# Kernel optimization log

Measured on AMD Instinct MI355X. Metric: run time of the kernel, lower is better.

## Reference

```python
import jax, jax.numpy as jnp
import numpy as np

K = 12
ORDERS = [(1, 2, 3), (1, 3, 2), (3, 2, 1), (3, 1, 2), (2, 1, 3), (2, 3, 1)]


def ranking_3d(x):
    # x: (B, L1, W1, H1, D) -> (B, 12, L1*W1*H1, D)
    B, L1, W1, H1, D = x.shape
    seqs = []
    for dims in ORDERS:
        perm = (0,) + dims + (4,)
        seqs.append(jnp.transpose(x, perm).reshape(B, -1, D))
        xr = jnp.flip(x, axis=dims)
        seqs.append(jnp.transpose(xr, perm).reshape(B, -1, D))
    return jnp.stack(seqs, axis=1)


def restore_original(out_y, shape):
    # out_y: (B, 12, D, L). NOTE: faithfully replicates the original code, which
    # reshapes the (B, D, L) slice directly to (B, d1, d2, d3, D).
    B, L1, W1, H1, D = shape
    size = {1: L1, 2: W1, 3: H1}
    restored = []
    for i in range(12):
        dims = ORDERS[i // 2]
        seq = out_y[:, i]  # (B, D, L)
        dims_shape = tuple(size[d] for d in dims)
        reshaped = seq.reshape((B,) + dims_shape + (D,))
        perm = (0,) + dims + (4,)
        inv = tuple(np.argsort(perm))
        r = jnp.transpose(reshaped, inv)
        if i % 2 == 1:
            r = jnp.flip(r, axis=dims)
        restored.append(r)
    return restored


def selective_scan(u, delta, A, Bs, Cs):
    # u, delta: (B,K,D,L); A: (K,D,N); Bs, Cs: (B,K,N,L)
    us = jnp.moveaxis(u, -1, 0)       # (L,B,K,D)
    ds = jnp.moveaxis(delta, -1, 0)   # (L,B,K,D)
    Bts = jnp.moveaxis(Bs, -1, 0)     # (L,B,K,N)
    Cts = jnp.moveaxis(Cs, -1, 0)     # (L,B,K,N)
    h0 = jnp.zeros(u.shape[:-1] + (A.shape[-1],), u.dtype)  # (B,K,D,N)

    def step(h, inp):
        ut, dt, Bt, Ct = inp
        dA = jnp.exp(dt[..., None] * A)                       # (B,K,D,N)
        h = dA * h + (dt * ut)[..., None] * Bt[:, :, None, :]
        y = jnp.einsum('bkdn,bkn->bkd', h, Ct)
        return h, y

    _, ys = jax.lax.scan(step, h0, (us, ds, Bts, Cts))
    return jnp.moveaxis(ys, 0, -1)  # (B,K,D,L)


def setup_inputs() -> dict:
    key = jax.random.key(0)
    ks = jax.random.split(key, 8)
    B, H, W, Len, D = 1, 16, 16, 16, 128
    N, R = 16, 8
    x = jax.random.normal(ks[0], (B, H, W, Len, D), dtype=jnp.float32)
    x_proj_weight = jax.random.normal(ks[1], (K, R + 2 * N, D), dtype=jnp.float32) * 0.02
    std = R ** -0.5
    dt_projs_weight = jax.random.uniform(ks[2], (K, D, R), minval=-std, maxval=std, dtype=jnp.float32)
    dt = jnp.exp(jax.random.uniform(ks[3], (K, D)) * (np.log(0.1) - np.log(0.001)) + np.log(0.001))
    dt = jnp.clip(dt, 1e-4, None)
    dt_projs_bias = (dt + jnp.log(-jnp.expm1(-dt))).astype(jnp.float32)
    A_logs = jnp.broadcast_to(jnp.log(jnp.arange(1, N + 1, dtype=jnp.float32)), (K, D, N)).copy()
    Ds = jnp.ones((K, D), dtype=jnp.float32)
    merge_w = jax.random.normal(ks[4], (K,), dtype=jnp.float32) * (1.0 / K)
    merge_b = jax.random.normal(ks[5], (), dtype=jnp.float32) * 0.01
    return {'x': x, 'x_proj_weight': x_proj_weight, 'dt_projs_weight': dt_projs_weight,
            'dt_projs_bias': dt_projs_bias, 'A_logs': A_logs, 'Ds': Ds,
            'merge_w': merge_w, 'merge_b': merge_b}


def reference(x, x_proj_weight, dt_projs_weight, dt_projs_bias, A_logs, Ds, merge_w, merge_b):
    B, H, W, Len, D = x.shape
    L = H * W * Len
    R = dt_projs_weight.shape[-1]
    N = A_logs.shape[-1]
    xs = jnp.transpose(ranking_3d(x), (0, 1, 3, 2))  # (B,K,D,L)
    x_dbl = jnp.einsum('bkdl,kcd->bkcl', xs, x_proj_weight)  # (B,K,R+2N,L)
    dts, Bs, Cs = jnp.split(x_dbl, [R, R + N], axis=2)
    dts = jnp.einsum('bkrl,kdr->bkdl', dts, dt_projs_weight)
    delta = jax.nn.softplus(dts + dt_projs_bias[None, :, :, None])
    A = -jnp.exp(A_logs)  # (K,D,N)
    ys = selective_scan(xs, delta, A, Bs, Cs)
    out_y = ys + Ds[None, :, :, None] * xs  # (B,K,D,L)
    restored = restore_original(out_y, (B, H, W, Len, D))
    stacked = jnp.stack(restored, axis=1)  # (B,K,H,W,Len,D)
    # mergeconv: 1x1 Conv2d over K channels == weighted sum across directions
    y = jnp.einsum('bkhwld,k->bhwld', stacked, merge_w) + merge_b
    return y
```

## Files before the change

### kernel.cpp

```cpp
#include <hip/hip_runtime.h>

#define KK 12
#define LL 4096
#define DD 128
#define NN 16
#define RR 8
#define NC 64
#define LC 64
#define XST 132
#define YST 66
#define SDST 44
#define XDBL_TILE (64 * SDST)

__device__ __forceinline__ int pos_of(int k, int l) {
    int o = k >> 1;
    int le = (k & 1) ? (4095 - l) : l;
    int t1 = le >> 8, t2 = (le >> 4) & 15, t3 = le & 15;
    switch (o) {
        case 0:  return (t1 << 8) | (t2 << 4) | t3;
        case 1:  return (t1 << 8) | (t3 << 4) | t2;
        case 2:  return (t3 << 8) | (t2 << 4) | t1;
        case 3:  return (t2 << 8) | (t3 << 4) | t1;
        case 4:  return (t2 << 8) | (t1 << 4) | t3;
        default: return (t3 << 8) | (t1 << 4) | t2;
    }
}

__device__ __forceinline__ float softplus_f(float z) {
    return fmaxf(z, 0.0f) + __logf(1.0f + __expf(-fabsf(z)));
}

__device__ __forceinline__ float delta_at(const float* sdbl, int i,
                                          float4 w0, float4 w1, float bz) {
    const float4* dr = (const float4*)(sdbl + i * SDST);
    float4 r0 = dr[0], r1 = dr[1];
    float z = bz + w0.x * r0.x + w0.y * r0.y + w0.z * r0.z + w0.w * r0.w
                 + w1.x * r1.x + w1.y * r1.y + w1.z * r1.z + w1.w * r1.w;
    return softplus_f(z);
}

__device__ __forceinline__ void e8_vec(bool structured, int half, float tl,
                                       float A0, const float* A8, float* e) {
    if (structured) {
        float q = __expf(tl * A0);
        float q2 = q * q, q4 = q2 * q2, q8 = q4 * q4;
        e[0] = half ? q8 * q : q;
        #pragma unroll
        for (int j = 1; j < 8; j++) e[j] = e[j - 1] * q;
    } else {
        #pragma unroll
        for (int j = 0; j < 8; j++) e[j] = __expf(tl * A8[j]);
    }
}

__device__ __forceinline__ bool load_A8(const float* __restrict__ A_logs,
                                        int k, int d, int n0, float* A8, float& A0) {
    const float4* ap = (const float4*)(A_logs + ((size_t)(k * DD + d) * NN + n0));
    float4 a0 = ap[0], a1 = ap[1];
    A8[0] = -__expf(a0.x); A8[1] = -__expf(a0.y);
    A8[2] = -__expf(a0.z); A8[3] = -__expf(a0.w);
    A8[4] = -__expf(a1.x); A8[5] = -__expf(a1.y);
    A8[6] = -__expf(a1.z); A8[7] = -__expf(a1.w);
    A0 = -__expf(A_logs[(size_t)(k * DD + d) * NN]);
    bool s = true;
    #pragma unroll
    for (int j = 0; j < 8; j++) {
        float m = (float)(n0 + j + 1);
        s = s && (fabsf(A8[j] - m * A0) <= 1e-4f * m * fabsf(A0));
    }
    return s;
}

__global__ __launch_bounds__(256) void k1_proj_scanA(
    const float* __restrict__ x, const float* __restrict__ Wp,
    const float* __restrict__ Wdt, const float* __restrict__ bias,
    const float* __restrict__ A_logs, const float* __restrict__ Ds,
    float* __restrict__ S, float* __restrict__ dtsum,
    float* __restrict__ oy, float* __restrict__ xdbl)
{
    const int blk = blockIdx.x;
    const int k = blk >> 6;
    const int c = blk & 63;
    const int l0 = c * LC;
    const int t = threadIdx.x;

    __shared__ float xs[64 * XST];
    __shared__ float sdbl[64 * SDST];
    __shared__ int   pos_s[64];

    if (t < 64) pos_s[t] = pos_of(k, l0 + t);
    __syncthreads();

    {
        int lane32 = t & 31, rowi = t >> 5;
        #pragma unroll
        for (int p = 0; p < 8; p++) {
            int l = p * 8 + rowi;
            float4 v = *(const float4*)(x + (size_t)pos_s[l] * DD + lane32 * 4);
            *(float4*)(&xs[l * XST + lane32 * 4]) = v;
        }
    }
    __syncthreads();

    {
        int l = t & 63, cgch = t >> 6;
        float acc[10];
        #pragma unroll
        for (int j = 0; j < 10; j++) acc[j] = 0.0f;
        const float* wk = Wp + (size_t)(k * 40 + cgch * 10) * DD;
        for (int d4 = 0; d4 < DD; d4 += 4) {
            float4 xv = *(const float4*)(&xs[l * XST + d4]);
            #pragma unroll
            for (int j = 0; j < 10; j++) {
                const float* w = wk + j * DD + d4;
                acc[j] += xv.x * w[0] + xv.y * w[1] + xv.z * w[2] + xv.w * w[3];
            }
        }
        #pragma unroll
        for (int j = 0; j < 10; j++) sdbl[l * SDST + cgch * 10 + j] = acc[j];
    }
    __syncthreads();

    if (c != 0) {
        for (int idx = t; idx < XDBL_TILE; idx += 256)
            xdbl[(size_t)blk * XDBL_TILE + idx] = sdbl[idx];
    }

    const int d = t >> 1, half = t & 1, n0 = half * 8;
    float A8[8], A0;
    bool structured = load_A8(A_logs, k, d, n0, A8, A0);
    const float4* wp4 = (const float4*)(Wdt + (size_t)(k * DD + d) * RR);
    const float4 w0 = wp4[0], w1 = wp4[1];
    const float bz = bias[k * DD + d];
    const float Dval = Ds[k * DD + d];
    float* ybuf = xs;

    {
        float h[8] = {0, 0, 0, 0, 0, 0, 0, 0};
        float dsum = 0.0f;
        #pragma unroll 4
        for (int i = 0; i < LC; i++) {
            float tl = delta_at(sdbl, i, w0, w1, bz);
            dsum += tl;
            float u = x[(size_t)pos_s[i] * DD + d];
            const float4* bp = (const float4*)(&sdbl[i * SDST + 8 + n0]);
            float4 b0 = bp[0], b1 = bp[1];
            const float4* cp = (const float4*)(&sdbl[i * SDST + 24 + n0]);
            float4 c0 = cp[0], c1 = cp[1];
            float e[8];
            e8_vec(structured, half, tl, A0, A8, e);
            float tu = tl * u;
            h[0] = e[0] * h[0] + tu * b0.x;  h[1] = e[1] * h[1] + tu * b0.y;
            h[2] = e[2] * h[2] + tu * b0.z;  h[3] = e[3] * h[3] + tu * b0.w;
            h[4] = e[4] * h[4] + tu * b1.x;  h[5] = e[5] * h[5] + tu * b1.y;
            h[6] = e[6] * h[6] + tu * b1.z;  h[7] = e[7] * h[7] + tu * b1.w;
            float yp = h[0] * c0.x + h[1] * c0.y + h[2] * c0.z + h[3] * c0.w
                     + h[4] * c1.x + h[5] * c1.y + h[6] * c1.z + h[7] * c1.w;
            float y = yp + __shfl_xor(yp, 1);
            if (!half) ybuf[d * YST + i] = y + Dval * u;
        }
        float4* sp = (float4*)(S + (((size_t)(k * NC + c) * DD + d) * NN + n0));
        sp[0] = make_float4(h[0], h[1], h[2], h[3]);
        sp[1] = make_float4(h[4], h[5], h[6], h[7]);
        if (!half) dtsum[(k * NC + c) * DD + d] = dsum;
    }
    __syncthreads();

    {
        int row = t >> 4, col = (t & 15) * 4;
        #pragma unroll
        for (int p = 0; p < 8; p++) {
            int r = p * 16 + row;
            float4 v = *(const float4*)(&ybuf[r * YST + col]);
            *(float4*)(oy + ((size_t)(k * DD + r)) * LL + l0 + col) = v;
        }
    }
}

__global__ __launch_bounds__(256) void k2_combine(
    float* __restrict__ S, const float* __restrict__ dtsum,
    const float* __restrict__ A_logs)
{
    int tid = blockIdx.x * 256 + threadIdx.x;
    int kk = tid >> 11, rem = tid & 2047, dd2 = rem >> 4;
    float Ac = -__expf(A_logs[tid]);
    float hh = 0.0f;
    #pragma unroll 8
    for (int c2 = 0; c2 < NC; c2++) {
        size_t base = ((size_t)(kk * NC + c2)) * 2048 + rem;
        float s = S[base];
        float dsv = dtsum[(kk * NC + c2) * DD + dd2];
        S[base] = hh;
        hh = s + __expf(dsv * Ac) * hh;
    }
}

__global__ __launch_bounds__(256) void k3_corr(
    const float* __restrict__ Wdt, const float* __restrict__ bias,
    const float* __restrict__ A_logs, const float* __restrict__ S,
    const float* __restrict__ xdbl, float* __restrict__ oy)
{
    const int blk = blockIdx.x;
    const int k = blk >> 6;
    const int c = blk & 63;
    if (c == 0) return;
    const int l0 = c * LC;
    const int t = threadIdx.x;

    __shared__ float sdbl[64 * SDST];
    __shared__ float ybuf[128 * YST];

    for (int idx = t; idx < XDBL_TILE; idx += 256)
        sdbl[idx] = xdbl[(size_t)blk * XDBL_TILE + idx];
    for (int idx = t; idx < 128 * YST; idx += 256)
        ybuf[idx] = 0.0f;
    __syncthreads();

    const int d = t >> 1, half = t & 1, n0 = half * 8;
    float A8[8], A0;
    bool structured = load_A8(A_logs, k, d, n0, A8, A0);
    const float4* wp4 = (const float4*)(Wdt + (size_t)(k * DD + d) * RR);
    const float4 w0 = wp4[0], w1 = wp4[1];
    const float bz = bias[k * DD + d];

    float corr[8];
    {
        const float4* hp = (const float4*)(S + (((size_t)(k * NC + c) * DD + d) * NN + n0));
        float4 h40 = hp[0], h41 = hp[1];
        corr[0] = h40.x; corr[1] = h40.y; corr[2] = h40.z; corr[3] = h40.w;
        corr[4] = h41.x; corr[5] = h41.y; corr[6] = h41.z; corr[7] = h41.w;
    }

    bool alive = true;
    for (int ii = 0; ii < 8 && alive; ii++) {
        #pragma unroll
        for (int jj = 0; jj < 8; jj++) {
            int i = ii * 8 + jj;
            float tl = delta_at(sdbl, i, w0, w1, bz);
            float e[8];
            e8_vec(structured, half, tl, A0, A8, e);
            #pragma unroll
            for (int j = 0; j < 8; j++) corr[j] *= e[j];
            const float4* cp = (const float4*)(&sdbl[i * SDST + 24 + n0]);
            float4 c0 = cp[0], c1 = cp[1];
            float yp = corr[0] * c0.x + corr[1] * c0.y + corr[2] * c0.z + corr[3] * c0.w
                     + corr[4] * c1.x + corr[5] * c1.y + corr[6] * c1.z + corr[7] * c1.w;
            float y = yp + __shfl_xor(yp, 1);
            if (!half) ybuf[d * YST + i] = y;
        }
        float mag = fabsf(corr[0]) + fabsf(corr[1]) + fabsf(corr[2]) + fabsf(corr[3])
                  + fabsf(corr[4]) + fabsf(corr[5]) + fabsf(corr[6]) + fabsf(corr[7]);
        if (__all(mag == 0.0f)) alive = false;
    }
    __syncthreads();

    {
        int row = t >> 4, col = (t & 15) * 4;
        #pragma unroll
        for (int p = 0; p < 8; p++) {
            int r = p * 16 + row;
            float4* addr = (float4*)(oy + ((size_t)(k * DD + r)) * LL + l0 + col);
            float4 v = *addr;
            const float4 w = *(const float4*)(&ybuf[r * YST + col]);
            v.x += w.x; v.y += w.y; v.z += w.z; v.w += w.w;
            *addr = v;
        }
    }
}

__global__ __launch_bounds__(256) void k4_merge(
    const float* __restrict__ out_y, const float* __restrict__ mw,
    const float* __restrict__ mb, float* __restrict__ out)
{
    int idx = blockIdx.x * 256 + threadIdx.x;
    int dd = idx & 127;
    int p = idx >> 7;
    int i3 = p & 15, i2 = (p >> 4) & 15, i1 = (p >> 8) & 15;

    float accv = mb[0];
    #pragma unroll
    for (int k = 0; k < 12; k++) {
        int a1 = i1, a2 = i2, a3 = i3;
        if (k & 1) { a1 = 15 - i1; a2 = 15 - i2; a3 = 15 - i3; }
        int j1, j2, j3;
        switch (k >> 1) {
            case 0:  j1 = a1; j2 = a2; j3 = a3; break;
            case 1:  j1 = a1; j2 = a3; j3 = a2; break;
            case 2:  j1 = a3; j2 = a2; j3 = a1; break;
            case 3:  j1 = a3; j2 = a1; j3 = a2; break;
            case 4:  j1 = a2; j2 = a1; j3 = a3; break;
            default: j1 = a2; j2 = a3; j3 = a1; break;
        }
        int jb = (j1 << 8) | (j2 << 4) | j3;
        accv += mw[k] * out_y[(size_t)k * (DD * LL) + (jb >> 5) * LL
                              + ((jb & 31) << 7) + dd];
    }
    out[idx] = accv;
}

extern "C" void kernel_launch(void* const* d_in, const int* in_sizes, int n_in,
                              void* d_out, int out_size, void* d_ws, size_t ws_size,
                              hipStream_t stream) {
    const float* x      = (const float*)d_in[0];
    const float* Wp     = (const float*)d_in[1];
    const float* Wdt    = (const float*)d_in[2];
    const float* bias   = (const float*)d_in[3];
    const float* A_logs = (const float*)d_in[4];
    const float* Ds     = (const float*)d_in[5];
    const float* mw     = (const float*)d_in[6];
    const float* mb     = (const float*)d_in[7];
    float* out = (float*)d_out;

    float* ws   = (float*)d_ws;
    float* S    = ws;
    float* dts  = S + (size_t)KK * NC * DD * NN;
    float* oy   = dts + (size_t)KK * NC * DD;
    float* xdbl = oy + (size_t)KK * DD * LL;

    k1_proj_scanA<<<dim3(KK * NC), dim3(256), 0, stream>>>(
        x, Wp, Wdt, bias, A_logs, Ds, S, dts, oy, xdbl);
    k2_combine<<<dim3(KK * DD * NN / 256), dim3(256), 0, stream>>>(S, dts, A_logs);
    k3_corr<<<dim3(KK * NC), dim3(256), 0, stream>>>(Wdt, bias, A_logs, S, xdbl, oy);
    k4_merge<<<dim3(LL * DD / 256), dim3(256), 0, stream>>>(oy, mw, mb, out);
}
```

Before: 179.3 us.

## Template scan kernels on structured A, keep outputs in registers, closed-form correction

The scan and correction kernels become templated on whether A is structured, so the per-step branch disappears and the 64-step loops fully unroll. Each thread pair keeps its half of the y outputs in registers and writes them straight to global memory, removing the shared-memory y buffer and its extra barrier. The scan now reads u from the shared x tile instead of global memory. The correction kernel computes exp(cumulative delta * A) * h0 in closed form, which removes the serial multiply chain and the early-exit test but puts an exp on every step. Launch bounds now request minimum occupancy, and copies use float4, at the risk of register spills from the larger unrolled bodies.

```diff
diff --git a/kernel.cpp b/kernel.cpp
--- a/kernel.cpp
+++ b/kernel.cpp
@@ -8,7 +8,6 @@
 #define NC 64
 #define LC 64
 #define XST 132
-#define YST 66
 #define SDST 44
 #define XDBL_TILE (64 * SDST)
 
@@ -26,31 +25,12 @@
     }
 }
 
-__device__ __forceinline__ float softplus_f(float z) {
-    return fmaxf(z, 0.0f) + __logf(1.0f + __expf(-fabsf(z)));
-}
-
-__device__ __forceinline__ float delta_at(const float* sdbl, int i,
-                                          float4 w0, float4 w1, float bz) {
+__device__ __forceinline__ float delta_row_z(const float* sdbl, int i,
+                                             float4 w0, float4 w1, float bz) {
     const float4* dr = (const float4*)(sdbl + i * SDST);
     float4 r0 = dr[0], r1 = dr[1];
-    float z = bz + w0.x * r0.x + w0.y * r0.y + w0.z * r0.z + w0.w * r0.w
-                 + w1.x * r1.x + w1.y * r1.y + w1.z * r1.z + w1.w * r1.w;
-    return softplus_f(z);
-}
-
-__device__ __forceinline__ void e8_vec(bool structured, int half, float tl,
-                                       float A0, const float* A8, float* e) {
-    if (structured) {
-        float q = __expf(tl * A0);
-        float q2 = q * q, q4 = q2 * q2, q8 = q4 * q4;
-        e[0] = half ? q8 * q : q;
-        #pragma unroll
-        for (int j = 1; j < 8; j++) e[j] = e[j - 1] * q;
-    } else {
-        #pragma unroll
-        for (int j = 0; j < 8; j++) e[j] = __expf(tl * A8[j]);
-    }
+    return bz + w0.x * r0.x + w0.y * r0.y + w0.z * r0.z + w0.w * r0.w
+              + w1.x * r1.x + w1.y * r1.y + w1.z * r1.z + w1.w * r1.w;
 }
 
 __device__ __forceinline__ bool load_A8(const float* __restrict__ A_logs,
@@ -71,11 +51,74 @@
     return s;
 }
 
-__global__ __launch_bounds__(256) void k1_proj_scanA(
+template<bool S>
+__device__ __forceinline__ void e8_from(float v, float A0, const float* A8,
+                                        int half, float* e) {
+    if (S) {
+        float q = __expf(v * A0);
+        float q2 = q * q, q4 = q2 * q2, q8 = q4 * q4;
+        e[0] = half ? q8 * q : q;
+        #pragma unroll
+        for (int j = 1; j < 8; j++) e[j] = e[j - 1] * q;
+    } else {
+        #pragma unroll
+        for (int j = 0; j < 8; j++) e[j] = __expf(v * A8[j]);
+    }
+}
+
+template<bool S>
+__device__ __forceinline__ void scanA_body(
+    const float* xs, const float* sdbl, int k, int c, int l0,
+    int d, int half, int n0, const float* A8, float A0,
+    float4 w0, float4 w1, float bz, float Dval,
+    float* __restrict__ S_g, float* __restrict__ dtsum,
+    float* __restrict__ oy)
+{
+    float h[8] = {0, 0, 0, 0, 0, 0, 0, 0};
+    float ybr[32];
+    float dsum = 0.0f;
+
+    #pragma unroll
+    for (int i = 0; i < LC; i++) {
+        float z = delta_row_z(sdbl, i, w0, w1, bz);
+        float E = __expf(-fabsf(z));
+        float dt = fmaxf(z, 0.0f) + __logf(1.0f + E);
+        float u = xs[i * XST + d];
+        dsum += dt;
+        float tu = dt * u;
+        float e[8];
+        e8_from<S>(dt, A0, A8, half, e);
+        const float4* bp = (const float4*)(&sdbl[i * SDST + 8 + n0]);
+        float4 b0 = bp[0], b1 = bp[1];
+        const float4* cp = (const float4*)(&sdbl[i * SDST + 24 + n0]);
+        float4 c0 = cp[0], c1 = cp[1];
+        h[0] = e[0] * h[0] + tu * b0.x;  h[1] = e[1] * h[1] + tu * b0.y;
+        h[2] = e[2] * h[2] + tu * b0.z;  h[3] = e[3] * h[3] + tu * b0.w;
+        h[4] = e[4] * h[4] + tu * b1.x;  h[5] = e[5] * h[5] + tu * b1.y;
+        h[6] = e[6] * h[6] + tu * b1.z;  h[7] = e[7] * h[7] + tu * b1.w;
+        float yp = h[0] * c0.x + h[1] * c0.y + h[2] * c0.z + h[3] * c0.w
+                 + h[4] * c1.x + h[5] * c1.y + h[6] * c1.z + h[7] * c1.w;
+        float yv = yp + __shfl_xor(yp, 1) + Dval * u;
+        if ((i >> 5) == half) ybr[i & 31] = yv;
+    }
+
+    float4* sp = (float4*)(S_g + (((size_t)(k * NC + c) * DD + d) * NN + n0));
+    sp[0] = make_float4(h[0], h[1], h[2], h[3]);
+    sp[1] = make_float4(h[4], h[5], h[6], h[7]);
+    if (!half) dtsum[(k * NC + c) * DD + d] = dsum;
+
+    float* base = oy + ((size_t)(k * DD + d)) * LL + l0 + half * 32;
+    #pragma unroll
+    for (int j = 0; j < 8; j++)
+        *(float4*)(base + j * 4) = make_float4(ybr[4*j], ybr[4*j+1],
+                                               ybr[4*j+2], ybr[4*j+3]);
+}
+
+__global__ __launch_bounds__(256, 3) void k1_proj_scanA(
     const float* __restrict__ x, const float* __restrict__ Wp,
     const float* __restrict__ Wdt, const float* __restrict__ bias,
     const float* __restrict__ A_logs, const float* __restrict__ Ds,
-    float* __restrict__ S, float* __restrict__ dtsum,
+    float* __restrict__ S_g, float* __restrict__ dtsum,
     float* __restrict__ oy, float* __restrict__ xdbl)
 {
     const int blk = blockIdx.x;
@@ -84,9 +127,9 @@
     const int l0 = c * LC;
     const int t = threadIdx.x;
 
-    __shared__ float xs[64 * XST];
-    __shared__ float sdbl[64 * SDST];
-    __shared__ int   pos_s[64];
+    __shared__ __align__(16) float xs[64 * XST];
+    __shared__ __align__(16) float sdbl[64 * SDST];
+    __shared__ int pos_s[64];
 
     if (t < 64) pos_s[t] = pos_of(k, l0 + t);
     __syncthreads();
@@ -122,8 +165,9 @@
     __syncthreads();
 
     if (c != 0) {
-        for (int idx = t; idx < XDBL_TILE; idx += 256)
-            xdbl[(size_t)blk * XDBL_TILE + idx] = sdbl[idx];
+        const float4* s4 = (const float4*)sdbl;
+        float4* g4 = (float4*)(xdbl + (size_t)blk * XDBL_TILE);
+        for (int idx = t; idx < XDBL_TILE / 4; idx += 256) g4[idx] = s4[idx];
     }
 
     const int d = t >> 1, half = t & 1, n0 = half * 8;
@@ -133,52 +177,17 @@
     const float4 w0 = wp4[0], w1 = wp4[1];
     const float bz = bias[k * DD + d];
     const float Dval = Ds[k * DD + d];
-    float* ybuf = xs;
-
-    {
-        float h[8] = {0, 0, 0, 0, 0, 0, 0, 0};
-        float dsum = 0.0f;
-        #pragma unroll 4
-        for (int i = 0; i < LC; i++) {
-            float tl = delta_at(sdbl, i, w0, w1, bz);
-            dsum += tl;
-            float u = x[(size_t)pos_s[i] * DD + d];
-            const float4* bp = (const float4*)(&sdbl[i * SDST + 8 + n0]);
-            float4 b0 = bp[0], b1 = bp[1];
-            const float4* cp = (const float4*)(&sdbl[i * SDST + 24 + n0]);
-            float4 c0 = cp[0], c1 = cp[1];
-            float e[8];
-            e8_vec(structured, half, tl, A0, A8, e);
-            float tu = tl * u;
-            h[0] = e[0] * h[0] + tu * b0.x;  h[1] = e[1] * h[1] + tu * b0.y;
-            h[2] = e[2] * h[2] + tu * b0.z;  h[3] = e[3] * h[3] + tu * b0.w;
-            h[4] = e[4] * h[4] + tu * b1.x;  h[5] = e[5] * h[5] + tu * b1.y;
-            h[6] = e[6] * h[6] + tu * b1.z;  h[7] = e[7] * h[7] + tu * b1.w;
-            float yp = h[0] * c0.x + h[1] * c0.y + h[2] * c0.z + h[3] * c0.w
-                     + h[4] * c1.x + h[5] * c1.y + h[6] * c1.z + h[7] * c1.w;
-            float y = yp + __shfl_xor(yp, 1);
-            if (!half) ybuf[d * YST + i] = y + Dval * u;
-        }
-        float4* sp = (float4*)(S + (((size_t)(k * NC + c) * DD + d) * NN + n0));
-        sp[0] = make_float4(h[0], h[1], h[2], h[3]);
-        sp[1] = make_float4(h[4], h[5], h[6], h[7]);
-        if (!half) dtsum[(k * NC + c) * DD + d] = dsum;
-    }
-    __syncthreads();
-
-    {
-        int row = t >> 4, col = (t & 15) * 4;
-        #pragma unroll
-        for (int p = 0; p < 8; p++) {
-            int r = p * 16 + row;
-            float4 v = *(const float4*)(&ybuf[r * YST + col]);
-            *(float4*)(oy + ((size_t)(k * DD + r)) * LL + l0 + col) = v;
-        }
-    }
+
+    if (structured)
+        scanA_body<true>(xs, sdbl, k, c, l0, d, half, n0, A8, A0, w0, w1, bz,
+                         Dval, S_g, dtsum, oy);
+    else
+        scanA_body<false>(xs, sdbl, k, c, l0, d, half, n0, A8, A0, w0, w1, bz,
+                          Dval, S_g, dtsum, oy);
 }
 
 __global__ __launch_bounds__(256) void k2_combine(
-    float* __restrict__ S, const float* __restrict__ dtsum,
+    float* __restrict__ S_g, const float* __restrict__ dtsum,
     const float* __restrict__ A_logs)
 {
     int tid = blockIdx.x * 256 + threadIdx.x;
@@ -188,16 +197,50 @@
     #pragma unroll 8
     for (int c2 = 0; c2 < NC; c2++) {
         size_t base = ((size_t)(kk * NC + c2)) * 2048 + rem;
-        float s = S[base];
+        float s = S_g[base];
         float dsv = dtsum[(kk * NC + c2) * DD + dd2];
-        S[base] = hh;
+        S_g[base] = hh;
         hh = s + __expf(dsv * Ac) * hh;
     }
 }
 
-__global__ __launch_bounds__(256) void k3_corr(
+template<bool S>
+__device__ __forceinline__ void corr_body(
+    const float* sdbl, int k, int c, int l0, int d, int half, int n0,
+    const float* A8, float A0, const float* h0,
+    float4 w0, float4 w1, float bz, float* __restrict__ oy)
+{
+    float ybr[32];
+    float Dsum = 0.0f;
+
+    #pragma unroll
+    for (int i = 0; i < LC; i++) {
+        float z = delta_row_z(sdbl, i, w0, w1, bz);
+        float E = __expf(-fabsf(z));
+        float dt = fmaxf(z, 0.0f) + __logf(1.0f + E);
+        Dsum += dt;
+        float e[8];
+        e8_from<S>(Dsum, A0, A8, half, e);
+        const float4* cp = (const float4*)(&sdbl[i * SDST + 24 + n0]);
+        float4 c0 = cp[0], c1 = cp[1];
+        float yp = e[0]*h0[0]*c0.x + e[1]*h0[1]*c0.y + e[2]*h0[2]*c0.z + e[3]*h0[3]*c0.w
+                 + e[4]*h0[4]*c1.x + e[5]*h0[5]*c1.y + e[6]*h0[6]*c1.z + e[7]*h0[7]*c1.w;
+        float yv = yp + __shfl_xor(yp, 1);
+        if ((i >> 5) == half) ybr[i & 31] = yv;
+    }
+
+    float* base = oy + ((size_t)(k * DD + d)) * LL + l0 + half * 32;
+    #pragma unroll
+    for (int j = 0; j < 8; j++) {
+        float4 v = *(float4*)(base + j * 4);
+        v.x += ybr[4*j]; v.y += ybr[4*j+1]; v.z += ybr[4*j+2]; v.w += ybr[4*j+3];
+        *(float4*)(base + j * 4) = v;
+    }
+}
+
+__global__ __launch_bounds__(256, 4) void k3_corr(
     const float* __restrict__ Wdt, const float* __restrict__ bias,
-    const float* __restrict__ A_logs, const float* __restrict__ S,
+    const float* __restrict__ A_logs, const float* __restrict__ S_g,
     const float* __restrict__ xdbl, float* __restrict__ oy)
 {
     const int blk = blockIdx.x;
@@ -207,13 +250,12 @@
     const int l0 = c * LC;
     const int t = threadIdx.x;
 
-    __shared__ float sdbl[64 * SDST];
-    __shared__ float ybuf[128 * YST];
-
-    for (int idx = t; idx < XDBL_TILE; idx += 256)
-        sdbl[idx] = xdbl[(size_t)blk * XDBL_TILE + idx];
-    for (int idx = t; idx < 128 * YST; idx += 256)
-        ybuf[idx] = 0.0f;
+    __shared__ __align__(16) float sdbl[64 * SDST];
+    {
+        const float4* g4 = (const float4*)(xdbl + (size_t)blk * XDBL_TILE);
+        float4* s4 = (float4*)sdbl;
+        for (int idx = t; idx < XDBL_TILE / 4; idx += 256) s4[idx] = g4[idx];
+    }
     __syncthreads();
 
     const int d = t >> 1, half = t & 1, n0 = half * 8;
@@ -223,49 +265,18 @@
     const float4 w0 = wp4[0], w1 = wp4[1];
     const float bz = bias[k * DD + d];
 
-    float corr[8];
+    float h0[8];
     {
-        const float4* hp = (const float4*)(S + (((size_t)(k * NC + c) * DD + d) * NN + n0));
+        const float4* hp = (const float4*)(S_g + (((size_t)(k * NC + c) * DD + d) * NN + n0));
         float4 h40 = hp[0], h41 = hp[1];
-        corr[0] = h40.x; corr[1] = h40.y; corr[2] = h40.z; corr[3] = h40.w;
-        corr[4] = h41.x; corr[5] = h41.y; corr[6] = h41.z; corr[7] = h41.w;
-    }
-
-    bool alive = true;
-    for (int ii = 0; ii < 8 && alive; ii++) {
-        #pragma unroll
-        for (int jj = 0; jj < 8; jj++) {
-            int i = ii * 8 + jj;
-            float tl = delta_at(sdbl, i, w0, w1, bz);
-            float e[8];
-            e8_vec(structured, half, tl, A0, A8, e);
-            #pragma unroll
-            for (int j = 0; j < 8; j++) corr[j] *= e[j];
-            const float4* cp = (const float4*)(&sdbl[i * SDST + 24 + n0]);
-            float4 c0 = cp[0], c1 = cp[1];
-            float yp = corr[0] * c0.x + corr[1] * c0.y + corr[2] * c0.z + corr[3] * c0.w
-                     + corr[4] * c1.x + corr[5] * c1.y + corr[6] * c1.z + corr[7] * c1.w;
-            float y = yp + __shfl_xor(yp, 1);
-            if (!half) ybuf[d * YST + i] = y;
-        }
-        float mag = fabsf(corr[0]) + fabsf(corr[1]) + fabsf(corr[2]) + fabsf(corr[3])
-                  + fabsf(corr[4]) + fabsf(corr[5]) + fabsf(corr[6]) + fabsf(corr[7]);
-        if (__all(mag == 0.0f)) alive = false;
-    }
-    __syncthreads();
-
-    {
-        int row = t >> 4, col = (t & 15) * 4;
-        #pragma unroll
-        for (int p = 0; p < 8; p++) {
-            int r = p * 16 + row;
-            float4* addr = (float4*)(oy + ((size_t)(k * DD + r)) * LL + l0 + col);
-            float4 v = *addr;
-            const float4 w = *(const float4*)(&ybuf[r * YST + col]);
-            v.x += w.x; v.y += w.y; v.z += w.z; v.w += w.w;
-            *addr = v;
-        }
-    }
+        h0[0] = h40.x; h0[1] = h40.y; h0[2] = h40.z; h0[3] = h40.w;
+        h0[4] = h41.x; h0[5] = h41.y; h0[6] = h41.z; h0[7] = h41.w;
+    }
+
+    if (structured)
+        corr_body<true>(sdbl, k, c, l0, d, half, n0, A8, A0, h0, w0, w1, bz, oy);
+    else
+        corr_body<false>(sdbl, k, c, l0, d, half, n0, A8, A0, h0, w0, w1, bz, oy);
 }
 
 __global__ __launch_bounds__(256) void k4_merge(
@@ -312,14 +323,14 @@
     float* out = (float*)d_out;
 
     float* ws   = (float*)d_ws;
-    float* S    = ws;
-    float* dts  = S + (size_t)KK * NC * DD * NN;
+    float* S_g  = ws;
+    float* dts  = S_g + (size_t)KK * NC * DD * NN;
     float* oy   = dts + (size_t)KK * NC * DD;
     float* xdbl = oy + (size_t)KK * DD * LL;
 
     k1_proj_scanA<<<dim3(KK * NC), dim3(256), 0, stream>>>(
-        x, Wp, Wdt, bias, A_logs, Ds, S, dts, oy, xdbl);
-    k2_combine<<<dim3(KK * DD * NN / 256), dim3(256), 0, stream>>>(S, dts, A_logs);
-    k3_corr<<<dim3(KK * NC), dim3(256), 0, stream>>>(Wdt, bias, A_logs, S, xdbl, oy);
+        x, Wp, Wdt, bias, A_logs, Ds, S_g, dts, oy, xdbl);
+    k2_combine<<<dim3(KK * DD * NN / 256), dim3(256), 0, stream>>>(S_g, dts, A_logs);
+    k3_corr<<<dim3(KK * NC), dim3(256), 0, stream>>>(Wdt, bias, A_logs, S_g, xdbl, oy);
     k4_merge<<<dim3(LL * DD / 256), dim3(256), 0, stream>>>(oy, mw, mb, out);
 }
```

Result: slower. 388.0 us (+116.4%).
